# Kernel tuning notes

Hardware: AMD Instinct MI355X
Metric: run time of the kernel (lower is better)

The kernel has to match this reference:

```python
import jax, jax.numpy as jnp
import numpy as np
from jax import lax

D = 256
B, W = 16, 32


def setup_inputs() -> dict:
    key = jax.random.key(0)
    ks = jax.random.split(key, 5)
    x = jax.random.normal(ks[0], (B, D, W, W), dtype=jnp.float32)
    w_qkv = jax.random.normal(ks[1], (3 * D, D), dtype=jnp.float32) * (1.0 / np.sqrt(D))
    b_qkv = jax.random.normal(ks[2], (3 * D,), dtype=jnp.float32) * 0.01
    w_out = jax.random.normal(ks[3], (D, D, 3, 3), dtype=jnp.float32) * (1.0 / np.sqrt(9 * D))
    b_out = jax.random.normal(ks[4], (D,), dtype=jnp.float32) * 0.01
    alpha = jnp.ones((), dtype=jnp.float32)
    return {"x": x, "w_qkv": w_qkv, "b_qkv": b_qkv, "w_out": w_out, "b_out": b_out, "alpha": alpha}


def reference(x, w_qkv, b_qkv, w_out, b_out, alpha):
    Bb, C, H, Ww = x.shape  # C == D, H == Ww
    N = H * Ww
    # 1x1 conv qkv projection
    qkv = jnp.einsum('bchw,oc->bohw', x, w_qkv) + b_qkv[None, :, None, None]
    q, k, v = jnp.split(qkv, 3, axis=1)
    q = q.reshape(Bb, C, N)
    k = k.reshape(Bb, C, N)
    v = v.reshape(Bb, C, N)
    scale = 1.0 / (C ** 0.5)
    attn = jax.nn.softmax(jnp.einsum('bcq,bck->bqk', q, k) * scale, axis=-1)  # [B,N,N]
    # faithful to torch: (B,N,C) memory-reinterpreted to (B,C,H,W)
    out = jnp.einsum('bqk,bck->bqc', attn, v).reshape(Bb, C, H, Ww)
    x = x + alpha * jax.nn.relu(out)
    conv = lax.conv_general_dilated(
        x, w_out, window_strides=(1, 1), padding='SAME',
        dimension_numbers=('NCHW', 'OIHW', 'NCHW')) + b_out[None, :, None, None]
    x = x + alpha * jax.nn.relu(conv)
    return x
```

## Files before the change

kernel.cpp:

```cpp
#include <hip/hip_runtime.h>
#include <cmath>

namespace {

constexpr int Dc  = 256;
constexpr int NB  = 16;
constexpr int NSP = 1024;
constexpr int OC3 = 768;

typedef __attribute__((ext_vector_type(8))) short  short8;
typedef __attribute__((ext_vector_type(8))) ushort ushort8;
typedef __attribute__((ext_vector_type(4))) ushort ushort4_v;
typedef __attribute__((ext_vector_type(4))) float  f32x4;

__device__ inline ushort f2bf(float f) {
  unsigned u = __builtin_bit_cast(unsigned, f);
  unsigned r = (u + 0x7FFFu + ((u >> 16) & 1u)) >> 16;
  return (ushort)r;
}
__device__ inline float bf2f(ushort u) {
  return __builtin_bit_cast(float, (unsigned)u << 16);
}

__device__ __forceinline__ void dma16(const ushort* g, ushort* l) {
  __builtin_amdgcn_global_load_lds(
      (const __attribute__((address_space(1))) unsigned int*)(const void*)g,
      (__attribute__((address_space(3))) unsigned int*)(void*)l, 16, 0, 0);
}

template<int BM>
__device__ __forceinline__ void mfma_core(
    const ushort* __restrict__ Abase, int lda,
    const ushort* __restrict__ Bbase, int ldb,
    int m0, int n0, int K, f32x4 (&acc)[BM / 32][4])
{
  constexpr int MI    = BM / 32;
  constexpr int AI    = BM / 64;
  constexpr int NLOAD = AI + 2;
  constexpr int BUFSZ = BM * 32 + 128 * 32;
  __shared__ ushort LDS[3 * BUFSZ];

  const int t = threadIdx.x;
  const int lane = t & 63, wid = t >> 6;
  const int wm = (wid >> 1) * (BM / 2);
  const int wo = (wid & 1) * 64;
  const int lm = lane & 15, lk = lane >> 4;
  const int aph = lk ^ ((lm >> 1) & 3);

  const int lrow = lane >> 2;
  const int niter = K >> 5;

  auto issue = [&](int kk) {
    const int c0 = kk << 5;
    ushort* buf = &LDS[(kk % 3) * BUFSZ];
#pragma unroll
    for (int i = 0; i < AI; ++i) {
      const int r0 = (i * 4 + wid) * 16;
      const int row = r0 + lrow;
      const int chunk = (lane & 3) ^ ((row >> 1) & 3);
      dma16(Abase + (size_t)(m0 + row) * lda + c0 + chunk * 8, buf + r0 * 32);
    }
#pragma unroll
    for (int i = 0; i < 2; ++i) {
      const int r0 = (i * 4 + wid) * 16;
      const int row = r0 + lrow;
      const int chunk = (lane & 3) ^ ((row >> 1) & 3);
      dma16(Bbase + (size_t)(n0 + row) * ldb + c0 + chunk * 8,
            buf + BM * 32 + r0 * 32);
    }
  };

  issue(0);
  issue(1);

  for (int kk = 0; kk < niter; ++kk) {
    __builtin_amdgcn_sched_barrier(0);
    if (kk < niter - 1) {
      if constexpr (NLOAD == 4)
        asm volatile("s_waitcnt vmcnt(4) lgkmcnt(0)" ::: "memory");
      else
        asm volatile("s_waitcnt vmcnt(3) lgkmcnt(0)" ::: "memory");
    } else {
      asm volatile("s_waitcnt vmcnt(0) lgkmcnt(0)" ::: "memory");
    }
    __builtin_amdgcn_s_barrier();
    __builtin_amdgcn_sched_barrier(0);
    if (kk + 2 < niter) issue(kk + 2);

    const ushort* Ab = &LDS[(kk % 3) * BUFSZ];
    const ushort* Bb = Ab + BM * 32;
    short8 af[MI], bw[4];
#pragma unroll
    for (int mi = 0; mi < MI; ++mi)
      af[mi] = *(const short8*)&Ab[(wm + mi * 16 + lm) * 32 + aph * 8];
#pragma unroll
    for (int oi = 0; oi < 4; ++oi)
      bw[oi] = *(const short8*)&Bb[(wo + oi * 16 + lm) * 32 + aph * 8];
#pragma unroll
    for (int mi = 0; mi < MI; ++mi)
#pragma unroll
      for (int oi = 0; oi < 4; ++oi)
        acc[mi][oi] = __builtin_amdgcn_mfma_f32_16x16x32_bf16(
            af[mi], bw[oi], acc[mi][oi], 0, 0, 0);
  }
}

__global__ __launch_bounds__(256) void k0w_wb(
    const float* __restrict__ w, ushort* __restrict__ wb,
    float* __restrict__ rowsum)
{
  const int i = blockIdx.x * 256 + threadIdx.x;
  wb[i] = f2bf(w[i]);
  if (i < NB * NSP) rowsum[i] = 0.0f;
}

__global__ __launch_bounds__(256) void k0x_xt(
    const float* __restrict__ x, ushort* __restrict__ xt)
{
  const int b  = blockIdx.z;
  const int c0 = blockIdx.y * 64;
  const int n0 = blockIdx.x * 64;
  __shared__ ushort tr[64][72];
  const int t = threadIdx.x;
  const float* xb = x + (size_t)b * Dc * NSP;
  const int nl4 = (t & 15) * 4, clb = t >> 4;
#pragma unroll
  for (int r = 0; r < 4; ++r) {
    const int cl = clb + r * 16;
    float4 xv = *(const float4*)(xb + (size_t)(c0 + cl) * NSP + n0 + nl4);
    tr[nl4 + 0][cl] = f2bf(xv.x);
    tr[nl4 + 1][cl] = f2bf(xv.y);
    tr[nl4 + 2][cl] = f2bf(xv.z);
    tr[nl4 + 3][cl] = f2bf(xv.w);
  }
  __syncthreads();
#pragma unroll
  for (int j = 0; j < 2; ++j) {
    const int s  = t + j * 256;
    const int nl = s >> 3, c8 = (s & 7) * 8;
    *(ushort8*)(xt + ((size_t)(b * NSP + n0 + nl)) * Dc + c0 + c8) =
        *(const ushort8*)&tr[nl][c8];
  }
}

__global__ __launch_bounds__(256) void k1a_qk(
    const ushort* __restrict__ wb, const ushort* __restrict__ xt,
    const float* __restrict__ b_qkv, ushort* __restrict__ qkt)
{
  const int b  = blockIdx.z;
  const int m0 = blockIdx.y * 128;
  const int n0 = blockIdx.x * 128;
  f32x4 acc[4][4];
#pragma unroll
  for (int i = 0; i < 4; ++i)
#pragma unroll
    for (int j = 0; j < 4; ++j) acc[i][j] = (f32x4)(0.0f);
  mfma_core<128>(wb, Dc, xt + (size_t)b * NSP * Dc, Dc, m0, n0, Dc, acc);
  const int t = threadIdx.x, lane = t & 63, wid = t >> 6;
  const int wm = (wid >> 1) * 64, wo = (wid & 1) * 64;
  const int lm = lane & 15, lk = lane >> 4;
  ushort* qb = qkt + (size_t)b * NSP * 512;
#pragma unroll
  for (int mi = 0; mi < 4; ++mi) {
    const int o = m0 + wm + mi * 16 + lk * 4;
    float4 bi = *(const float4*)(b_qkv + o);
#pragma unroll
    for (int oi = 0; oi < 4; ++oi) {
      const int n = n0 + wo + oi * 16 + lm;
      f32x4 a = acc[mi][oi];
      ushort4_v st = { f2bf(a.x + bi.x), f2bf(a.y + bi.y),
                       f2bf(a.z + bi.z), f2bf(a.w + bi.w) };
      *(ushort4_v*)(qb + (size_t)n * 512 + o) = st;
    }
  }
}

__global__ __launch_bounds__(256) void k1b_v(
    const ushort* __restrict__ wb, const ushort* __restrict__ xt,
    const float* __restrict__ b_qkv, ushort* __restrict__ vb)
{
  const int b  = blockIdx.z;
  const int m0 = blockIdx.y * 64;
  const int n0 = blockIdx.x * 128;
  f32x4 acc[2][4];
#pragma unroll
  for (int i = 0; i < 2; ++i)
#pragma unroll
    for (int j = 0; j < 4; ++j) acc[i][j] = (f32x4)(0.0f);
  mfma_core<64>(xt + (size_t)b * NSP * Dc, Dc, wb + 512 * Dc, Dc, m0, n0, Dc, acc);
  const int t = threadIdx.x, lane = t & 63, wid = t >> 6;
  const int wm = (wid >> 1) * 32, wo = (wid & 1) * 64;
  const int lm = lane & 15, lk = lane >> 4;
  ushort* vbb = vb + (size_t)b * Dc * NSP;
#pragma unroll
  for (int oi = 0; oi < 4; ++oi) {
    const int c = n0 + wo + oi * 16 + lm;
    const float bo = b_qkv[512 + c];
#pragma unroll
    for (int mi = 0; mi < 2; ++mi) {
      const int n = m0 + wm + mi * 16 + lk * 4;
      f32x4 a = acc[mi][oi];
      ushort4_v st = { f2bf(a.x + bo), f2bf(a.y + bo),
                       f2bf(a.z + bo), f2bf(a.w + bo) };
      *(ushort4_v*)(vbb + (size_t)c * NSP + n) = st;
    }
  }
}

__global__ __launch_bounds__(256) void k2m_exp(
    const ushort* __restrict__ qkt, ushort* __restrict__ E,
    float* __restrict__ rowsum)
{
  const int b  = blockIdx.z;
  const int m0 = blockIdx.y * 128;
  const int n0 = blockIdx.x * 128;
  const ushort* base = qkt + (size_t)b * NSP * 512;
  f32x4 acc[4][4];
#pragma unroll
  for (int i = 0; i < 4; ++i)
#pragma unroll
    for (int j = 0; j < 4; ++j) acc[i][j] = (f32x4)(0.0f);
  mfma_core<128>(base + 256, 512, base, 512, m0, n0, Dc, acc);
  const int t = threadIdx.x, lane = t & 63, wid = t >> 6;
  const int wm = (wid >> 1) * 64, wo = (wid & 1) * 64;
  const int lm = lane & 15, lk = lane >> 4;
  ushort* Eb = E + (size_t)b * NSP * NSP;
  float* rs = rowsum + (size_t)b * NSP;
#pragma unroll
  for (int oi = 0; oi < 4; ++oi) {
    const int q = n0 + wo + oi * 16 + lm;
    float ps = 0.0f;
#pragma unroll
    for (int mi = 0; mi < 4; ++mi) {
      const int kidx = m0 + wm + mi * 16 + lk * 4;
      f32x4 a = acc[mi][oi] * 0.0625f;
      float e0 = __expf(a.x), e1 = __expf(a.y);
      float e2 = __expf(a.z), e3 = __expf(a.w);
      ps += (e0 + e1) + (e2 + e3);
      ushort4_v st = { f2bf(e0), f2bf(e1), f2bf(e2), f2bf(e3) };
      *(ushort4_v*)(Eb + (size_t)q * NSP + kidx) = st;
    }
    ps += __shfl_xor(ps, 16);
    ps += __shfl_xor(ps, 32);
    if (lane < 16) atomicAdd(rs + q, ps);
  }
}

__global__ __launch_bounds__(256) void k4f_pv(
    const ushort* __restrict__ vb, const ushort* __restrict__ E,
    const float* __restrict__ rowsum, const float* __restrict__ x,
    const float* __restrict__ alphap, ushort* __restrict__ x1p)
{
  const int b  = blockIdx.z;
  const int m0 = blockIdx.y * 64;
  const int n0 = blockIdx.x * 128;
  f32x4 acc[2][4];
#pragma unroll
  for (int i = 0; i < 2; ++i)
#pragma unroll
    for (int j = 0; j < 4; ++j) acc[i][j] = (f32x4)(0.0f);
  mfma_core<64>(vb + (size_t)b * Dc * NSP, NSP,
                E + (size_t)b * NSP * NSP, NSP, m0, n0, NSP, acc);

  __shared__ float T[64][133];
  const int t = threadIdx.x, lane = t & 63, wid = t >> 6;
  const int wm = (wid >> 1) * 32, wo = (wid & 1) * 64;
  const int lm = lane & 15, lk = lane >> 4;
  const float* rs = rowsum + (size_t)b * NSP;
#pragma unroll
  for (int oi = 0; oi < 4; ++oi) {
    const int ql = wo + oi * 16 + lm;
    const float inv = 1.0f / rs[n0 + ql];
#pragma unroll
    for (int mi = 0; mi < 2; ++mi) {
      const int cl = wm + mi * 16 + lk * 4;
      f32x4 a = acc[mi][oi] * inv;
      T[cl + 0][ql] = a.x;
      T[cl + 1][ql] = a.y;
      T[cl + 2][ql] = a.z;
      T[cl + 3][ql] = a.w;
    }
  }
  __syncthreads();

  const float al = *alphap;
  const int s = wid;
  const int c_off = lane;
  const int sp = s * 256 + m0 + c_off;
  const int r34 = ((sp >> 5) + 1) * 34 + (sp & 31) + 1;
  const int ch0 = n0 >> 2;
  const float* xb32 = x + (size_t)b * Dc * NSP;
  ushort* xpb = x1p + (size_t)b * 1156 * 256;
  ushort8 pack[4];
#pragma unroll
  for (int g = 0; g < 4; ++g) {
#pragma unroll
    for (int e = 0; e < 8; ++e) {
      const int chl = g * 8 + e;
      const float v  = T[c_off][4 * chl + s];
      const float xv = xb32[(size_t)(ch0 + chl) * NSP + sp];
      pack[g][e] = f2bf(xv + al * fmaxf(v, 0.f));
    }
  }
  ushort8* dst = (ushort8*)(xpb + (size_t)r34 * 256 + ch0);
#pragma unroll
  for (int g = 0; g < 4; ++g) dst[g] = pack[g];
}

__global__ __launch_bounds__(256) void k0_wt(
    const float* __restrict__ w_out, ushort* __restrict__ w2b)
{
  const int o  = blockIdx.x;
  const int ic = threadIdx.x;
  const float* src = w_out + ((size_t)o * Dc + ic) * 9;
#pragma unroll
  for (int k9 = 0; k9 < 9; ++k9)
    w2b[((size_t)k9 * Dc + o) * Dc + ic] = f2bf(src[k9]);
}

__global__ __launch_bounds__(256) void k5z_border(ushort* __restrict__ x1p)
{
  const int b = blockIdx.x;
  ushort* p = x1p + (size_t)b * 1156 * 256;
  const int t = threadIdx.x;
  for (int r = 0; r < 132; ++r) {
    int r34;
    if (r < 34)      r34 = r;
    else if (r < 68) r34 = 33 * 34 + (r - 34);
    else { const int rr = r - 68; r34 = (1 + (rr >> 1)) * 34 + (rr & 1) * 33; }
    p[(size_t)r34 * 256 + t] = 0;
  }
}

__global__ __launch_bounds__(256) void k6_conv_mfma(
    const ushort* __restrict__ x1p, const ushort* __restrict__ w2b,
    const float* __restrict__ bout, const float* __restrict__ alphap,
    float* __restrict__ out)
{
  const int b  = blockIdx.z;
  const int n0 = blockIdx.x * 64;
  const int o0 = blockIdx.y * 128;
  __shared__ ushort LDS[3 * 12288];
  const int t = threadIdx.x;
  const int lane = t & 63, wid = t >> 6;
  const int wm = (wid >> 1) * 32, wo = (wid & 1) * 64;
  const int lm = lane & 15, lk = lane >> 4;
  const int aphr = lm & 7;

  const int lrow   = wid * 8 + (lane >> 3);
  const int lchunk = ((lane & 7) ^ (lane >> 3)) * 8;

  const ushort* xp = x1p + (size_t)b * 1156 * 256;
  const int nA0 = n0 + lrow;
  const int r34A0 = ((nA0 >> 5) + 1) * 34 + (nA0 & 31) + 1;
  const ushort* Ag0 = xp + (size_t)r34A0 * 256 + lchunk;
  const ushort* Ag1 = Ag0 + (size_t)34 * 256;
  const ushort* Wg  = w2b + (size_t)(o0 + lrow) * 256 + lchunk;

  auto issue = [&](int kt) {
    const int buf = kt % 3;
    const int k9 = kt >> 2;
    const int dh = ((k9 * 11) >> 5) - 1;
    const int dw = k9 - (dh + 1) * 3 - 1;
    const int aoff = (dh * 34 + dw) * 256 + ((kt & 3) << 6);
    const size_t woff = (size_t)k9 * 65536 + ((kt & 3) << 6);
    ushort* lb = &LDS[buf * 12288 + wid * 512];
    dma16(Ag0 + aoff, lb);
    dma16(Ag1 + aoff, lb + 2048);
#pragma unroll
    for (int i = 0; i < 4; ++i)
      dma16(Wg + woff + i * 8192, lb + 4096 + i * 2048);
  };

  f32x4 acc[2][4];
#pragma unroll
  for (int i = 0; i < 2; ++i)
#pragma unroll
    for (int j = 0; j < 4; ++j) acc[i][j] = (f32x4)(0.0f);

  issue(0);
  issue(1);

  for (int kt = 0; kt < 36; ++kt) {
    __builtin_amdgcn_sched_barrier(0);
    if (kt < 35)
      asm volatile("s_waitcnt vmcnt(6) lgkmcnt(0)" ::: "memory");
    else
      asm volatile("s_waitcnt vmcnt(0) lgkmcnt(0)" ::: "memory");
    __builtin_amdgcn_s_barrier();
    __builtin_amdgcn_sched_barrier(0);
    if (kt + 2 < 36) issue(kt + 2);

    const ushort* Ab = &LDS[(kt % 3) * 12288];
    const ushort* Wb = Ab + 4096;
#pragma unroll
    for (int s = 0; s < 2; ++s) {
      const int ph = ((s << 2) | lk) ^ aphr;
      short8 af[2], bw[4];
#pragma unroll
      for (int mi = 0; mi < 2; ++mi)
        af[mi] = *(const short8*)&Ab[(wm + mi * 16 + lm) * 64 + ph * 8];
#pragma unroll
      for (int oi = 0; oi < 4; ++oi)
        bw[oi] = *(const short8*)&Wb[(wo + oi * 16 + lm) * 64 + ph * 8];
#pragma unroll
      for (int mi = 0; mi < 2; ++mi)
#pragma unroll
        for (int oi = 0; oi < 4; ++oi)
          acc[mi][oi] = __builtin_amdgcn_mfma_f32_16x16x32_bf16(
              af[mi], bw[oi], acc[mi][oi], 0, 0, 0);
    }
  }

  const float al = *alphap;
  float* ob = out + (size_t)b * Dc * NSP;
#pragma unroll
  for (int oi = 0; oi < 4; ++oi) {
    const int o = o0 + wo + oi * 16 + lm;
    const float bo = bout[o];
#pragma unroll
    for (int mi = 0; mi < 2; ++mi) {
      const int nr = n0 + wm + mi * 16 + lk * 4;
      const int r34 = ((nr >> 5) + 1) * 34 + (nr & 31) + 1;
      const ushort* xr = xp + (size_t)r34 * 256 + o;
      f32x4 a = acc[mi][oi];
      float4 r;
      r.x = bf2f(xr[0])   + al * fmaxf(a.x + bo, 0.f);
      r.y = bf2f(xr[256]) + al * fmaxf(a.y + bo, 0.f);
      r.z = bf2f(xr[512]) + al * fmaxf(a.z + bo, 0.f);
      r.w = bf2f(xr[768]) + al * fmaxf(a.w + bo, 0.f);
      *(float4*)(ob + (size_t)o * NSP + nr) = r;
    }
  }
}

}

extern "C" void kernel_launch(void* const* d_in, const int* in_sizes, int n_in,
                              void* d_out, int out_size, void* d_ws, size_t ws_size,
                              hipStream_t stream)
{
  const float* x     = (const float*)d_in[0];
  const float* w_qkv = (const float*)d_in[1];
  const float* b_qkv = (const float*)d_in[2];
  const float* w_out = (const float*)d_in[3];
  const float* b_out = (const float*)d_in[4];
  const float* alpha = (const float*)d_in[5];
  float* out = (float*)d_out;

  char* ws = (char*)d_ws;
  ushort* qkt  = (ushort*)ws;
  ushort* x1p  = (ushort*)ws;
  ushort* vb   = (ushort*)(ws + (16u << 20));
  ushort* xt   = (ushort*)(ws + (24u << 20));
  ushort* w2b  = xt;
  ushort* wb   = (ushort*)(ws + (32u << 20));
  float*  rowsum = (float*)(ws + (32u << 20) + (1u << 19));
  ushort* E    = (ushort*)(ws + (33u << 20));

  k0w_wb      <<<dim3(768),        256, 0, stream>>>(w_qkv, wb, rowsum);
  k0x_xt      <<<dim3(16, 4, 16),  256, 0, stream>>>(x, xt);
  k1a_qk      <<<dim3(8, 4, 16),   256, 0, stream>>>(wb, xt, b_qkv, qkt);
  k1b_v       <<<dim3(2, 16, 16),  256, 0, stream>>>(wb, xt, b_qkv, vb);
  k0_wt       <<<dim3(256),        256, 0, stream>>>(w_out, w2b);
  k2m_exp     <<<dim3(8, 8, 16),   256, 0, stream>>>(qkt, E, rowsum);
  k5z_border  <<<dim3(16),         256, 0, stream>>>(x1p);
  k4f_pv      <<<dim3(8, 4, 16),   256, 0, stream>>>(vb, E, rowsum, x, alpha, x1p);
  k6_conv_mfma<<<dim3(16, 2, 16),  256, 0, stream>>>(x1p, w2b, b_out, alpha, out);
}
```

Baseline: 110.7 us.

## Merge prep kernels into one launch and read bf16 residual in PV epilogue

Four small preprocessing kernels (weight casts, x transpose, conv weight reorder, padded border zeroing) are merged into one launch dispatched by block index, and the workspace is rearranged so w2b and x1p get their own regions instead of aliasing xt and qkt. The PV epilogue now reads the residual x from the bf16 transposed copy with contiguous 16-byte loads instead of strided fp32 reads. This cuts launch overhead and epilogue memory traffic. The cost is that the residual in x1p is rounded to bf16 before the add, not after.

```diff
diff --git a/kernel.cpp b/kernel.cpp
--- a/kernel.cpp
+++ b/kernel.cpp
@@ -105,41 +105,69 @@
   }
 }
 
-__global__ __launch_bounds__(256) void k0w_wb(
-    const float* __restrict__ w, ushort* __restrict__ wb,
-    float* __restrict__ rowsum)
-{
-  const int i = blockIdx.x * 256 + threadIdx.x;
-  wb[i] = f2bf(w[i]);
-  if (i < NB * NSP) rowsum[i] = 0.0f;
-}
-
-__global__ __launch_bounds__(256) void k0x_xt(
-    const float* __restrict__ x, ushort* __restrict__ xt)
-{
-  const int b  = blockIdx.z;
-  const int c0 = blockIdx.y * 64;
-  const int n0 = blockIdx.x * 64;
+__global__ __launch_bounds__(256) void k0_prep(
+    const float* __restrict__ x, const float* __restrict__ w_qkv,
+    const float* __restrict__ w_out,
+    ushort* __restrict__ xt, ushort* __restrict__ wb,
+    ushort* __restrict__ w2b, float* __restrict__ rowsum,
+    ushort* __restrict__ x1p)
+{
   __shared__ ushort tr[64][72];
+  int bid = blockIdx.x;
   const int t = threadIdx.x;
-  const float* xb = x + (size_t)b * Dc * NSP;
-  const int nl4 = (t & 15) * 4, clb = t >> 4;
-#pragma unroll
-  for (int r = 0; r < 4; ++r) {
-    const int cl = clb + r * 16;
-    float4 xv = *(const float4*)(xb + (size_t)(c0 + cl) * NSP + n0 + nl4);
-    tr[nl4 + 0][cl] = f2bf(xv.x);
-    tr[nl4 + 1][cl] = f2bf(xv.y);
-    tr[nl4 + 2][cl] = f2bf(xv.z);
-    tr[nl4 + 3][cl] = f2bf(xv.w);
-  }
-  __syncthreads();
-#pragma unroll
-  for (int j = 0; j < 2; ++j) {
-    const int s  = t + j * 256;
-    const int nl = s >> 3, c8 = (s & 7) * 8;
-    *(ushort8*)(xt + ((size_t)(b * NSP + n0 + nl)) * Dc + c0 + c8) =
-        *(const ushort8*)&tr[nl][c8];
+  if (bid < 768) {
+    const int i = bid * 256 + t;
+    wb[i] = f2bf(w_qkv[i]);
+    if (i < NB * NSP) rowsum[i] = 0.0f;
+    return;
+  }
+  bid -= 768;
+  if (bid < 1024) {
+    const int b  = bid >> 6;
+    const int r  = bid & 63;
+    const int c0 = (r >> 4) * 64;
+    const int n0 = (r & 15) * 64;
+    const float* xb = x + (size_t)b * Dc * NSP;
+    const int nl4 = (t & 15) * 4, clb = t >> 4;
+#pragma unroll
+    for (int rr = 0; rr < 4; ++rr) {
+      const int cl = clb + rr * 16;
+      float4 xv = *(const float4*)(xb + (size_t)(c0 + cl) * NSP + n0 + nl4);
+      tr[nl4 + 0][cl] = f2bf(xv.x);
+      tr[nl4 + 1][cl] = f2bf(xv.y);
+      tr[nl4 + 2][cl] = f2bf(xv.z);
+      tr[nl4 + 3][cl] = f2bf(xv.w);
+    }
+    __syncthreads();
+#pragma unroll
+    for (int j = 0; j < 2; ++j) {
+      const int s  = t + j * 256;
+      const int nl = s >> 3, c8 = (s & 7) * 8;
+      *(ushort8*)(xt + ((size_t)(b * NSP + n0 + nl)) * Dc + c0 + c8) =
+          *(const ushort8*)&tr[nl][c8];
+    }
+    return;
+  }
+  bid -= 1024;
+  if (bid < 256) {
+    const int o  = bid;
+    const int ic = t;
+    const float* src = w_out + ((size_t)o * Dc + ic) * 9;
+#pragma unroll
+    for (int k9 = 0; k9 < 9; ++k9)
+      w2b[((size_t)k9 * Dc + o) * Dc + ic] = f2bf(src[k9]);
+    return;
+  }
+  bid -= 256;
+  {
+    ushort* p = x1p + (size_t)bid * 1156 * 256;
+    for (int r = 0; r < 132; ++r) {
+      int r34;
+      if (r < 34)      r34 = r;
+      else if (r < 68) r34 = 33 * 34 + (r - 34);
+      else { const int rr = r - 68; r34 = (1 + (rr >> 1)) * 34 + (rr & 1) * 33; }
+      p[(size_t)r34 * 256 + t] = 0;
+    }
   }
 }
 
@@ -248,7 +276,7 @@
 
 __global__ __launch_bounds__(256) void k4f_pv(
     const ushort* __restrict__ vb, const ushort* __restrict__ E,
-    const float* __restrict__ rowsum, const float* __restrict__ x,
+    const float* __restrict__ rowsum, const ushort* __restrict__ xt,
     const float* __restrict__ alphap, ushort* __restrict__ x1p)
 {
   const int b  = blockIdx.z;
@@ -289,47 +317,22 @@
   const int sp = s * 256 + m0 + c_off;
   const int r34 = ((sp >> 5) + 1) * 34 + (sp & 31) + 1;
   const int ch0 = n0 >> 2;
-  const float* xb32 = x + (size_t)b * Dc * NSP;
+  const ushort* xtb = xt + (size_t)b * NSP * Dc + (size_t)sp * Dc + ch0;
   ushort* xpb = x1p + (size_t)b * 1156 * 256;
   ushort8 pack[4];
 #pragma unroll
   for (int g = 0; g < 4; ++g) {
+    ushort8 xv = *(const ushort8*)(xtb + g * 8);
 #pragma unroll
     for (int e = 0; e < 8; ++e) {
       const int chl = g * 8 + e;
-      const float v  = T[c_off][4 * chl + s];
-      const float xv = xb32[(size_t)(ch0 + chl) * NSP + sp];
-      pack[g][e] = f2bf(xv + al * fmaxf(v, 0.f));
+      const float v = T[c_off][4 * chl + s];
+      pack[g][e] = f2bf(bf2f(xv[e]) + al * fmaxf(v, 0.f));
     }
   }
   ushort8* dst = (ushort8*)(xpb + (size_t)r34 * 256 + ch0);
 #pragma unroll
   for (int g = 0; g < 4; ++g) dst[g] = pack[g];
-}
-
-__global__ __launch_bounds__(256) void k0_wt(
-    const float* __restrict__ w_out, ushort* __restrict__ w2b)
-{
-  const int o  = blockIdx.x;
-  const int ic = threadIdx.x;
-  const float* src = w_out + ((size_t)o * Dc + ic) * 9;
-#pragma unroll
-  for (int k9 = 0; k9 < 9; ++k9)
-    w2b[((size_t)k9 * Dc + o) * Dc + ic] = f2bf(src[k9]);
-}
-
-__global__ __launch_bounds__(256) void k5z_border(ushort* __restrict__ x1p)
-{
-  const int b = blockIdx.x;
-  ushort* p = x1p + (size_t)b * 1156 * 256;
-  const int t = threadIdx.x;
-  for (int r = 0; r < 132; ++r) {
-    int r34;
-    if (r < 34)      r34 = r;
-    else if (r < 68) r34 = 33 * 34 + (r - 34);
-    else { const int rr = r - 68; r34 = (1 + (rr >> 1)) * 34 + (rr & 1) * 33; }
-    p[(size_t)r34 * 256 + t] = 0;
-  }
 }
 
 __global__ __launch_bounds__(256) void k6_conv_mfma(
@@ -450,21 +453,19 @@
 
   char* ws = (char*)d_ws;
   ushort* qkt  = (ushort*)ws;
-  ushort* x1p  = (ushort*)ws;
   ushort* vb   = (ushort*)(ws + (16u << 20));
   ushort* xt   = (ushort*)(ws + (24u << 20));
-  ushort* w2b  = xt;
   ushort* wb   = (ushort*)(ws + (32u << 20));
   float*  rowsum = (float*)(ws + (32u << 20) + (1u << 19));
   ushort* E    = (ushort*)(ws + (33u << 20));
-
-  k0w_wb      <<<dim3(768),        256, 0, stream>>>(w_qkv, wb, rowsum);
-  k0x_xt      <<<dim3(16, 4, 16),  256, 0, stream>>>(x, xt);
+  ushort* w2b  = (ushort*)(ws + (65u << 20));
+  ushort* x1p  = (ushort*)(ws + (67u << 20));
+
+  k0_prep     <<<dim3(2064),       256, 0, stream>>>(x, w_qkv, w_out,
+                                                     xt, wb, w2b, rowsum, x1p);
   k1a_qk      <<<dim3(8, 4, 16),   256, 0, stream>>>(wb, xt, b_qkv, qkt);
   k1b_v       <<<dim3(2, 16, 16),  256, 0, stream>>>(wb, xt, b_qkv, vb);
-  k0_wt       <<<dim3(256),        256, 0, stream>>>(w_out, w2b);
   k2m_exp     <<<dim3(8, 8, 16),   256, 0, stream>>>(qkt, E, rowsum);
-  k5z_border  <<<dim3(16),         256, 0, stream>>>(x1p);
-  k4f_pv      <<<dim3(8, 4, 16),   256, 0, stream>>>(vb, E, rowsum, x, alpha, x1p);
+  k4f_pv      <<<dim3(8, 4, 16),   256, 0, stream>>>(vb, E, rowsum, xt, alpha, x1p);
   k6_conv_mfma<<<dim3(16, 2, 16),  256, 0, stream>>>(x1p, w2b, b_out, alpha, out);
 }
```

New measurement: 102.4 us. 7.5% less time.
